# Optimization experiments

Measured on AMD Instinct MI355X. Metric: run time of the kernel, lower is better.

Reference implementation:

```python
import jax, jax.numpy as jnp
import numpy as np
import math

B = 2
LAYERS = 18
LATENT = 512
MAPPER_LAYER = 7  # w_code_num[attention_layer=11]
CLUSTERS = 10
CLUSTER_LAYER = 11
CLUSTER_DIM = 512 + 2 * (512 // 16)  # 576
LR_MUL = 0.1
LAYER_NUM = [0, 2, 3, 5, 6, 8, 9, 11, 12, 14, 15, 17, 18, 20, 21, 23, 24]
CH = [512] * 11 + [256] * 2 + [128] * 3 + [64] * 3 + [32] * 3 + [16] * 3
RES = [4, 8, 8, 16, 16, 32, 32, 64, 64, 128, 128] + [256] * 14


def _forward(x, fmaps, mw, mb, afw, afb, aw, ab, alw, alb, initial_state):
    batch = x.shape[0]
    blend = fmaps[CLUSTER_LAYER - 1]
    size = blend.shape[2]  # 128

    # ---- cluster assignment (torch.no_grad block) ----
    pc = blend.shape[1] // 16  # position_channel = 32
    coords = jnp.arange(size, dtype=jnp.float32) * (2.0 / (size - 1)) - 1.0
    xp = jnp.broadcast_to(coords[None, :], (size, size))
    yp = jnp.broadcast_to(coords[:, None], (size, size))
    cf = jnp.concatenate([
        blend,
        jnp.broadcast_to(xp[None, None], (batch, pc, size, size)),
        jnp.broadcast_to(yp[None, None], (batch, pc, size, size)),
    ], axis=1)
    cf = jax.lax.stop_gradient(cf)
    flat = cf.transpose(0, 2, 3, 1).reshape(-1, cf.shape[1])  # [B*S*S, 576]
    dis = (jnp.sum(flat * flat, axis=1, keepdims=True)
           - 2.0 * flat @ initial_state.T
           + jnp.sum(initial_state * initial_state, axis=1)[None, :])
    assign = jnp.argmin(dis, axis=1).reshape(batch, size, size)
    choice = jnp.arange(batch)[:, None, None] * CLUSTERS + assign  # [B,S,S]

    x7 = x[:, :MAPPER_LAYER, -LATENT:]
    h = x7 * jax.lax.rsqrt(jnp.mean(x7 * x7, axis=-1, keepdims=True) + 1e-8)
    w_scale = (1.0 / math.sqrt(LATENT)) * LR_MUL
    for i in range(3):
        h = jnp.einsum('bci,coi->bco', h, mw[:, i]) * w_scale
        h = jax.nn.leaky_relu(h + mb[:, i][None] * LR_MUL, 0.2) * math.sqrt(2.0)
    delta_zs = jnp.concatenate(
        [h, jnp.zeros((batch, LAYERS - MAPPER_LAYER, LATENT), h.dtype)], axis=1)
    loss_delta = jnp.mean(jnp.sqrt(jnp.sum(delta_zs[:, :MAPPER_LAYER] ** 2, axis=-1)))

    # ---- attention branch (EqualConv2d 1x1 + nearest interpolate, torch semantics) ----
    def conv1x1(f, w, b):
        cin = f.shape[1]
        return jnp.einsum('bihw,oi->bohw', f, w) * (1.0 / math.sqrt(cin)) + b[None, :, None, None]

    def interp(f):  # torch nearest: src = floor(i * in / out)
        H = f.shape[2]
        idx = (jnp.arange(size) * H) // size
        return f[:, :, idx][:, :, :, idx]

    att = [interp(conv1x1(fmaps[-1], afw, afb))]
    for c in range(LAYERS - 1):
        f = fmaps[LAYER_NUM[c]]
        att.append(interp(conv1x1(f, aw[c][:, :f.shape[1]], ab[c])))
    amap = jnp.concatenate(att, axis=1)  # [B, 32*18, S, S]
    logits = jnp.einsum('bihw,i->bhw', amap, alw) * (1.0 / math.sqrt(32 * LAYERS)) + alb[0]
    each = jax.nn.sigmoid(logits)  # [B,S,S]

    # ---- training branch: per-(batch,cluster) masked mean -> segment mean ----
    nseg = batch * CLUSTERS
    seg = choice.reshape(-1)
    vals = each.reshape(-1)
    sums = jax.ops.segment_sum(vals, seg, num_segments=nseg)
    cnts = jax.ops.segment_sum(jnp.ones_like(vals), seg, num_segments=nseg)
    mean = sums / jnp.maximum(cnts, 1.0)
    attention_map = jnp.where(cnts > 0, mean, 1.0)[choice]  # [B,S,S]
    loss_reg = jnp.sum(jnp.where(cnts > 0, jnp.maximum(mean - 0.8, 0.0), 0.0)) / batch
    loss_tv = jnp.mean((each - jax.lax.stop_gradient(attention_map)) ** 2)

    am = attention_map[:, None]  # [B,1,S,S]
    final = jnp.where(am < 0.8, am - jax.lax.stop_gradient(am), am)
    # torchvision gaussian_blur(k=5): sigma = 0.3*((5-1)*0.5-1)+0.8 = 1.1, reflect pad
    xs = jnp.linspace(-2.0, 2.0, 5)
    k1 = jnp.exp(-0.5 * (xs / 1.1) ** 2)
    k1 = k1 / jnp.sum(k1)
    k2 = jnp.outer(k1, k1)[None, None]  # [1,1,5,5]
    padded = jnp.pad(final, ((0, 0), (0, 0), (2, 2), (2, 2)), mode='reflect')
    blurred = jax.lax.conv_general_dilated(padded, k2.astype(final.dtype), (1, 1), 'VALID')
    return delta_zs, blurred, loss_delta, loss_reg, loss_tv


def setup_inputs() -> dict:
    key = jax.random.key(0)
    ks = jax.random.split(key, 40)
    inp = {}
    inp['x'] = jax.random.normal(ks[0], (B, LAYERS, LATENT), jnp.float32)
    for i in range(25):
        inp[f'fmap_{i}'] = jax.random.normal(ks[1 + i], (B, CH[i], RES[i], RES[i]), jnp.float32)
    inp['fmap_25'] = jax.random.normal(ks[26], (B, 512, 4, 4), jnp.float32)
    inp['mw'] = jax.random.normal(ks[27], (MAPPER_LAYER, 3, LATENT, LATENT), jnp.float32)
    inp['mb'] = 0.1 * jax.random.normal(ks[28], (MAPPER_LAYER, 3, LATENT), jnp.float32)
    inp['afw'] = jax.random.normal(ks[29], (32, 512), jnp.float32)
    inp['afb'] = 0.1 * jax.random.normal(ks[30], (32,), jnp.float32)
    inp['aw'] = jax.random.normal(ks[31], (LAYERS - 1, 32, 512), jnp.float32)
    inp['ab'] = 0.1 * jax.random.normal(ks[32], (LAYERS - 1, 32), jnp.float32)
    inp['alw'] = jax.random.normal(ks[33], (32 * LAYERS,), jnp.float32)
    inp['alb'] = jnp.full((1,), 5.0, jnp.float32)  # attention_last bias init to 5
    inp['initial_state'] = jax.random.normal(ks[34], (CLUSTERS, CLUSTER_DIM), jnp.float32)
    inp['size'] = 128
    return inp


def reference(x, fmap_0, fmap_1, fmap_2, fmap_3, fmap_4, fmap_5, fmap_6, fmap_7,
              fmap_8, fmap_9, fmap_10, fmap_11, fmap_12, fmap_13, fmap_14, fmap_15,
              fmap_16, fmap_17, fmap_18, fmap_19, fmap_20, fmap_21, fmap_22, fmap_23,
              fmap_24, fmap_25, mw, mb, afw, afb, aw, ab, alw, alb, initial_state, size):
    fmaps = [fmap_0, fmap_1, fmap_2, fmap_3, fmap_4, fmap_5, fmap_6, fmap_7, fmap_8,
             fmap_9, fmap_10, fmap_11, fmap_12, fmap_13, fmap_14, fmap_15, fmap_16,
             fmap_17, fmap_18, fmap_19, fmap_20, fmap_21, fmap_22, fmap_23, fmap_24,
             fmap_25]
    return _forward(x, fmaps, mw, mb, afw, afb, aw, ab, alw, alb, initial_state)
```

## Files before the change

### kernel.cpp

```cpp
#include <hip/hip_runtime.h>
#include <math.h>

#define NPIX 32768
#define OUT_DZ 0
#define OUT_BLUR 18432
#define OUT_LD 51200
#define OUT_REG 51201
#define OUT_TV 51202
#define NSLAB 48

__constant__ int d_cin[18] = {512,512,512,512,512,512,512,512,256,256,128,128,64,64,32,32,16,16};
__constant__ int d_H[18]   = {4,  4,  8,  16, 32, 32, 64, 128,256,256,256,256,256,256,256,256,256,256};

__constant__ int d_slab_t[NSLAB]  = {0,1,2,3,4,5, 6,6,
                                     7,7,7,7,7,7,7,7,
                                     8,8,8,8,8,8,8,8,
                                     9,9,9,9,9,9,9,9,
                                     10,10,10,10, 11,11,11,11,
                                     12,12, 13,13, 14, 15, 16, 17};
__constant__ int d_slab_c0[NSLAB] = {0,0,0,0,0,0, 0,256,
                                     0,64,128,192,256,320,384,448,
                                     0,32,64,96,128,160,192,224,
                                     0,32,64,96,128,160,192,224,
                                     0,32,64,96, 0,32,64,96,
                                     0,32, 0,32, 0, 0, 0, 0};
__constant__ int d_slab_nc[NSLAB] = {512,512,512,512,512,512, 256,256,
                                     64,64,64,64,64,64,64,64,
                                     32,32,32,32,32,32,32,32,
                                     32,32,32,32,32,32,32,32,
                                     32,32,32,32, 32,32,32,32,
                                     32,32, 32,32, 32, 32, 16, 16};

struct FPtrs { const float* f[18]; };

#define WS_HA     0
#define WS_HB     7168
#define WS_ST     14336
#define WS_CN     22528
#define WS_BIASP  22576
#define WS_V      22656
#define WS_CHOICE 31872
#define WS_PART   64640
#define WS_EACH   1637504
#define WS_SUMS   1670272
#define WS_CNTS   1672832
#define WS_ATTV   1675392
#define WS_TVP    1675424

__global__ __launch_bounds__(512) void k_vfold(
    const float* __restrict__ afw, const float* __restrict__ afb,
    const float* __restrict__ aw,  const float* __restrict__ ab,
    const float* __restrict__ alw, const float* __restrict__ istate,
    float* __restrict__ v, float* __restrict__ biasp,
    float* __restrict__ st, float* __restrict__ cn)
{
    int t = blockIdx.x;
    if (t < 18) {
        int cin = d_cin[t];
        const float* w  = (t==0) ? afw : aw + (size_t)(t-1)*32*512;
        const float* bb = (t==0) ? afb : ab + (t-1)*32;
        float scale = (1.0f/sqrtf((float)cin)) * (1.0f/24.0f);
        int c = threadIdx.x;
        if (c < cin) {
            float s = 0.0f;
            #pragma unroll 8
            for (int o = 0; o < 32; o++) s += alw[t*32+o] * w[o*512 + c];
            v[t*512 + c] = s * scale;
        }
        if (threadIdx.x == 0) {
            float s = 0.0f;
            for (int o = 0; o < 32; o++) s += alw[t*32+o] * bb[o];
            biasp[t] = s * (1.0f/24.0f);
        }
    } else {
        int c = threadIdx.x;
        if (c < 512) {
            #pragma unroll
            for (int j = 0; j < 10; j++) st[c*16 + j] = -2.0f * istate[j*576 + c];
        }
        if (c < 10) {
            int j = c;
            float n = 0.0f, s1 = 0.0f, s2 = 0.0f;
            for (int k = 0; k < 576; k++) { float sv = istate[j*576+k]; n += sv*sv; }
            for (int k = 512; k < 544; k++) s1 += istate[j*576+k];
            for (int k = 544; k < 576; k++) s2 += istate[j*576+k];
            cn[j] = n; cn[16+j] = -2.0f*s1; cn[32+j] = -2.0f*s2;
        }
    }
}

__global__ __launch_bounds__(512, 4) void k_assign(
    const float* __restrict__ blend, const float* __restrict__ st,
    const float* __restrict__ cn, int* __restrict__ choice)
{
    __shared__ float gsh[8*128*10];
    int tid = threadIdx.x;
    int w = tid >> 6, lane = tid & 63;
    int csub = __builtin_amdgcn_readfirstlane(w);
    int pw = blockIdx.x * 128;
    int b = pw >> 14, rem = pw & 16383;
    const float* src = blend + ((size_t)b*512 + csub*64)*16384 + rem + 2*lane;
    const float* stc = st + csub*64*16;
    float g0[10] = {0,0,0,0,0,0,0,0,0,0};
    float g1[10] = {0,0,0,0,0,0,0,0,0,0};
    for (int c0 = 0; c0 < 64; c0 += 4) {
        float2 q[4];
        #pragma unroll
        for (int u = 0; u < 4; u++) q[u] = *(const float2*)(src + (size_t)(c0+u)*16384);
        #pragma unroll
        for (int u = 0; u < 4; u++) {
            #pragma unroll
            for (int j = 0; j < 10; j++) {
                float sv = stc[(c0+u)*16 + j];
                g0[j] = fmaf(q[u].x, sv, g0[j]);
                g1[j] = fmaf(q[u].y, sv, g1[j]);
            }
        }
    }
    #pragma unroll
    for (int j = 0; j < 10; j++) {
        gsh[(w*128 + 2*lane)*10 + j]     = g0[j];
        gsh[(w*128 + 2*lane + 1)*10 + j] = g1[j];
    }
    __syncthreads();
    if (tid < 128) {
        int p = pw + tid;
        int bb = p >> 14, rr = p & 16383, y = rr >> 7, x = rr & 127;
        float cx = (float)x * (float)(2.0/127.0) - 1.0f;
        float cy = (float)y * (float)(2.0/127.0) - 1.0f;
        float gt[10];
        #pragma unroll
        for (int j = 0; j < 10; j++) {
            float acc = cn[j] + cn[16+j]*cx + cn[32+j]*cy;
            #pragma unroll
            for (int ww = 0; ww < 8; ww++) acc += gsh[(ww*128 + tid)*10 + j];
            gt[j] = acc;
        }
        int best = 0; float bg = gt[0];
        #pragma unroll
        for (int j = 1; j < 10; j++) if (gt[j] < bg) { bg = gt[j]; best = j; }
        choice[p] = bb*10 + best;
    }
}

__global__ __launch_bounds__(256) void k_norm(const float* __restrict__ x, float* __restrict__ h)
{
    int r = blockIdx.x;
    int b = r / 7, c = r % 7;
    const float* xr = x + ((size_t)b*18 + c)*512;
    int tid = threadIdx.x;
    float v0 = xr[tid], v1 = xr[tid+256];
    __shared__ float red[256];
    __shared__ float scale;
    red[tid] = v0*v0 + v1*v1; __syncthreads();
    for (int s = 128; s; s >>= 1) { if (tid < s) red[tid] += red[tid+s]; __syncthreads(); }
    if (tid == 0) scale = 1.0f / sqrtf(red[0]*(1.0f/512.0f) + 1e-8f);
    __syncthreads();
    h[r*512 + tid] = v0*scale; h[r*512 + 256 + tid] = v1*scale;
}

__global__ __launch_bounds__(256) void k_mlp(
    const float* __restrict__ mw, const float* __restrict__ mb,
    const float* __restrict__ hin, float* __restrict__ hout,
    int layer, float* __restrict__ dz)
{
    int wave = blockIdx.x*4 + (threadIdx.x >> 6);
    int lane = threadIdx.x & 63;
    int c = wave >> 9, o = wave & 511;
    const float* wrow = mw + (((size_t)(c*3 + layer)*512 + o) << 9) + lane*8;
    float4 w0 = *(const float4*)wrow;
    float4 w1 = *(const float4*)(wrow + 4);
    const float* h0 = hin + (size_t)c*512 + lane*8;
    const float* h1 = hin + (size_t)(7 + c)*512 + lane*8;
    float4 a0 = *(const float4*)h0, a1 = *(const float4*)(h0+4);
    float4 b0 = *(const float4*)h1, b1 = *(const float4*)(h1+4);
    float d0 = a0.x*w0.x + a0.y*w0.y + a0.z*w0.z + a0.w*w0.w
             + a1.x*w1.x + a1.y*w1.y + a1.z*w1.z + a1.w*w1.w;
    float d1 = b0.x*w0.x + b0.y*w0.y + b0.z*w0.z + b0.w*w0.w
             + b1.x*w1.x + b1.y*w1.y + b1.z*w1.z + b1.w*w1.w;
    #pragma unroll
    for (int m = 32; m; m >>= 1) { d0 += __shfl_xor(d0, m); d1 += __shfl_xor(d1, m); }
    if (lane == 0) {
        const float wsc = (float)(0.1/22.62741699796952);
        const float rt2 = 1.41421356237309515f;
        float bias = mb[(c*3 + layer)*512 + o] * 0.1f;
        float z0 = d0*wsc + bias; z0 = (z0 > 0.0f ? z0 : 0.2f*z0) * rt2;
        float z1 = d1*wsc + bias; z1 = (z1 > 0.0f ? z1 : 0.2f*z1) * rt2;
        hout[(size_t)c*512 + o] = z0;
        hout[(size_t)(7 + c)*512 + o] = z1;
        if (dz) {
            dz[((size_t)0*18 + c)*512 + o] = z0;
            dz[((size_t)1*18 + c)*512 + o] = z1;
        }
    }
}

__global__ __launch_bounds__(256) void k_lossdelta(const float* __restrict__ h, float* __restrict__ outp)
{
    __shared__ float red[256];
    int tid = threadIdx.x;
    float total = 0.0f;
    for (int r = 0; r < 14; r++) {
        float v0 = h[r*512 + tid], v1 = h[r*512 + 256 + tid];
        red[tid] = v0*v0 + v1*v1; __syncthreads();
        for (int s = 128; s; s >>= 1) { if (tid < s) red[tid] += red[tid+s]; __syncthreads(); }
        if (tid == 0) total += sqrtf(red[0]);
        __syncthreads();
    }
    if (tid == 0) outp[0] = total * (1.0f/14.0f);
}

__global__ __launch_bounds__(256) void k_zero(float* __restrict__ out)
{
    int z = blockIdx.x*256 + threadIdx.x;
    if (z < 11264) {
        int b = z / (11*512), rem = z % (11*512);
        out[(size_t)b*18*512 + 7*512 + rem] = 0.0f;
    }
}

__global__ __launch_bounds__(256, 4) void k_each(FPtrs fp, const float* __restrict__ v, float* __restrict__ partial)
{
    __shared__ float vsh[512];
    int bid = blockIdx.x;
    int tid = threadIdx.x;
    int s = (bid < 512) ? (bid >> 6) : (8 + ((bid - 512) >> 4));
    int t  = d_slab_t[s];
    int c0 = d_slab_c0[s];
    int nc = d_slab_nc[s];
    int H  = d_H[t];
    int cin = d_cin[t];
    for (int i = tid; i < nc; i += 256) vsh[i] = v[t*512 + c0 + i];
    __syncthreads();
    int w = tid >> 6, lane = tid & 63;

    if (bid >= 512) {
        int sub = (bid - 512) & 15;
        int b = sub >> 3, rowgrp = sub & 7;
        int y0 = rowgrp*16 + w*4;
        const float* base = fp.f[t] + (size_t)(b*cin + c0) * (size_t)H * (size_t)H;
        float* pout = partial + (size_t)s*NPIX + b*16384;
        if (H == 256) {
            float a[4][2] = {{0,0},{0,0},{0,0},{0,0}};
            const float* srcr[4];
            #pragma unroll
            for (int i = 0; i < 4; i++) srcr[i] = base + (size_t)(2*(y0+i))*256 + 4*lane;
            for (int cc = 0; cc < nc; cc += 2) {
                float4 q[2][4];
                #pragma unroll
                for (int u = 0; u < 2; u++)
                    #pragma unroll
                    for (int i = 0; i < 4; i++)
                        q[u][i] = *(const float4*)(srcr[i] + (size_t)(cc+u)*65536);
                #pragma unroll
                for (int u = 0; u < 2; u++) {
                    float vv = vsh[cc+u];
                    #pragma unroll
                    for (int i = 0; i < 4; i++) {
                        a[i][0] = fmaf(q[u][i].x, vv, a[i][0]);
                        a[i][1] = fmaf(q[u][i].z, vv, a[i][1]);
                    }
                }
            }
            #pragma unroll
            for (int i = 0; i < 4; i++) {
                float2 o; o.x = a[i][0]; o.y = a[i][1];
                *(float2*)(pout + (y0+i)*128 + 2*lane) = o;
            }
        } else {
            int h = lane >> 5, c4 = 4*(lane & 31);
            float aA[4] = {0,0,0,0}, aB[4] = {0,0,0,0};
            const float* srcA = base + (size_t)(y0 + h)*128 + c4;
            const float* srcB = base + (size_t)(y0 + 2 + h)*128 + c4;
            for (int cc = 0; cc < nc; cc += 4) {
                float4 qa[4], qb[4];
                #pragma unroll
                for (int u = 0; u < 4; u++) {
                    qa[u] = *(const float4*)(srcA + (size_t)(cc+u)*16384);
                    qb[u] = *(const float4*)(srcB + (size_t)(cc+u)*16384);
                }
                #pragma unroll
                for (int u = 0; u < 4; u++) {
                    float vv = vsh[cc+u];
                    aA[0] = fmaf(qa[u].x, vv, aA[0]); aA[1] = fmaf(qa[u].y, vv, aA[1]);
                    aA[2] = fmaf(qa[u].z, vv, aA[2]); aA[3] = fmaf(qa[u].w, vv, aA[3]);
                    aB[0] = fmaf(qb[u].x, vv, aB[0]); aB[1] = fmaf(qb[u].y, vv, aB[1]);
                    aB[2] = fmaf(qb[u].z, vv, aB[2]); aB[3] = fmaf(qb[u].w, vv, aB[3]);
                }
            }
            float4 oA; oA.x=aA[0]; oA.y=aA[1]; oA.z=aA[2]; oA.w=aA[3];
            float4 oB; oB.x=aB[0]; oB.y=aB[1]; oB.z=aB[2]; oB.w=aB[3];
            *(float4*)(pout + (y0+h)*128 + c4) = oA;
            *(float4*)(pout + (y0+2+h)*128 + c4) = oB;
        }
        return;
    }

    int px = bid & 63;
    int row = w, pbase = px*512;
    int b = pbase >> 14;
    int y = ((pbase & 16383) >> 7) + row;
    const float* base = fp.f[t] + (size_t)(b*cin + c0) * (size_t)(H*H);
    float a0 = 0.0f, a1 = 0.0f;
    if (H == 64) {
        const float* src = base + (size_t)(y >> 1)*64 + lane;
        for (int cc = 0; cc < nc; cc += 8) {
            float q[8];
            #pragma unroll
            for (int u = 0; u < 8; u++) q[u] = src[(size_t)(cc+u)*4096];
            #pragma unroll
            for (int u = 0; u < 8; u++) {
                float vv = vsh[cc+u];
                a0 = fmaf(q[u], vv, a0); a1 = fmaf(q[u], vv, a1);
            }
        }
    } else {
        int x0 = 2*lane, x1 = 2*lane + 1;
        int sy = (y*H) >> 7, sx0 = (x0*H) >> 7, sx1 = (x1*H) >> 7;
        const float* src = base + (size_t)sy*H;
        size_t HH = (size_t)H*H;
        for (int cc = 0; cc < nc; cc += 8) {
            float q0[8], q1[8];
            #pragma unroll
            for (int u = 0; u < 8; u++) {
                q0[u] = src[(size_t)(cc+u)*HH + sx0];
                q1[u] = src[(size_t)(cc+u)*HH + sx1];
            }
            #pragma unroll
            for (int u = 0; u < 8; u++) {
                float vv = vsh[cc+u];
                a0 = fmaf(q0[u], vv, a0); a1 = fmaf(q1[u], vv, a1);
            }
        }
    }
    int p = pbase + row*128 + 2*lane;
    float2 o; o.x = a0; o.y = a1;
    *(float2*)(partial + (size_t)s*NPIX + p) = o;
}

__global__ __launch_bounds__(256) void k_logits(
    const float* __restrict__ partial, const float* __restrict__ biasp,
    const float* __restrict__ alb, const int* __restrict__ choice,
    float* __restrict__ each, float* __restrict__ bsums, int* __restrict__ bcnts)
{
    __shared__ float ssum[20]; __shared__ int scnt[20]; __shared__ float sbias;
    int tid = threadIdx.x;
    if (tid < 20) { ssum[tid] = 0.0f; scnt[tid] = 0; }
    if (tid == 0) {
        float s = alb[0];
        for (int t = 0; t < 18; t++) s += biasp[t];
        sbias = s;
    }
    __syncthreads();
    int p = blockIdx.x*256 + tid;
    float lg = sbias;
    #pragma unroll 8
    for (int s = 0; s < NSLAB; s++) lg += partial[(size_t)s*NPIX + p];
    float e = 1.0f / (1.0f + expf(-lg));
    each[p] = e;
    int ch = choice[p];
    atomicAdd(&ssum[ch], e);
    atomicAdd(&scnt[ch], 1);
    __syncthreads();
    if (tid < 20) { bsums[blockIdx.x*20 + tid] = ssum[tid]; bcnts[blockIdx.x*20 + tid] = scnt[tid]; }
}

__global__ __launch_bounds__(64) void k_stats(
    const float* __restrict__ bsums, const int* __restrict__ bcnts,
    float* __restrict__ attv, float* __restrict__ out)
{
    __shared__ float red[32];
    int j = threadIdx.x;
    float regj = 0.0f;
    if (j < 20) {
        float s = 0.0f; int c = 0;
        for (int blk = 0; blk < 128; blk++) { s += bsums[blk*20 + j]; c += bcnts[blk*20 + j]; }
        float mean = s / fmaxf((float)c, 1.0f);
        attv[j] = (c > 0) ? mean : 1.0f;
        regj = (c > 0) ? fmaxf(mean - 0.8f, 0.0f) : 0.0f;
    }
    if (j < 32) red[j] = (j < 20) ? regj : 0.0f;
    __syncthreads();
    for (int s = 16; s; s >>= 1) { if (j < s) red[j] += red[j+s]; __syncthreads(); }
    if (j == 0) out[OUT_REG] = red[0] * 0.5f;
}

__global__ __launch_bounds__(256) void k_final(
    const float* __restrict__ each, const int* __restrict__ choice,
    const float* __restrict__ attv, float* __restrict__ tvp, float* __restrict__ out)
{
    __shared__ float av[20];
    __shared__ float red[256];
    int tid = threadIdx.x;
    if (tid < 20) av[tid] = attv[tid];
    __syncthreads();
    int p = blockIdx.x*256 + tid;
    int b = p >> 14, rem = p & 16383, y = rem >> 7, x = rem & 127;
    float k1[5]; float ks = 0.0f;
    #pragma unroll
    for (int i = 0; i < 5; i++) { float d = (float)(i-2) / 1.1f; k1[i] = expf(-0.5f*d*d); ks += k1[i]; }
    #pragma unroll
    for (int i = 0; i < 5; i++) k1[i] /= ks;
    const int* cb = choice + b*16384;
    float acc = 0.0f;
    #pragma unroll
    for (int a = 0; a < 5; a++) {
        int yy = y + a - 2; yy = (yy < 0) ? -yy : ((yy > 127) ? 254 - yy : yy);
        #pragma unroll
        for (int bb = 0; bb < 5; bb++) {
            int xx = x + bb - 2; xx = (xx < 0) ? -xx : ((xx > 127) ? 254 - xx : xx);
            float am = av[cb[yy*128 + xx]];
            float fin = (am < 0.8f) ? 0.0f : am;
            acc += k1[a]*k1[bb]*fin;
        }
    }
    out[OUT_BLUR + p] = acc;
    float amc = av[cb[y*128 + x]];
    float d = each[p] - amc;
    red[tid] = d*d; __syncthreads();
    for (int s = 128; s; s >>= 1) { if (tid < s) red[tid] += red[tid+s]; __syncthreads(); }
    if (tid == 0) tvp[blockIdx.x] = red[0];
}

__global__ __launch_bounds__(128) void k_tvred(const float* __restrict__ tvp, float* __restrict__ out)
{
    __shared__ float red[128];
    int tid = threadIdx.x;
    red[tid] = tvp[tid]; __syncthreads();
    for (int s = 64; s; s >>= 1) { if (tid < s) red[tid] += red[tid+s]; __syncthreads(); }
    if (tid == 0) out[OUT_TV] = red[0] * (1.0f/32768.0f);
}

extern "C" void kernel_launch(void* const* d_in, const int* in_sizes, int n_in,
                              void* d_out, int out_size, void* d_ws, size_t ws_size,
                              hipStream_t stream)
{
    const float* x      = (const float*)d_in[0];
    const float* blend  = (const float*)d_in[11];
    const float* mw     = (const float*)d_in[27];
    const float* mb     = (const float*)d_in[28];
    const float* afw    = (const float*)d_in[29];
    const float* afb    = (const float*)d_in[30];
    const float* aw     = (const float*)d_in[31];
    const float* ab     = (const float*)d_in[32];
    const float* alw    = (const float*)d_in[33];
    const float* alb    = (const float*)d_in[34];
    const float* istate = (const float*)d_in[35];
    float* out = (float*)d_out;
    float* ws  = (float*)d_ws;

    static const int LN[17] = {0,2,3,5,6,8,9,11,12,14,15,17,18,20,21,23,24};
    FPtrs fp;
    fp.f[0] = (const float*)d_in[26];
    for (int c = 0; c < 17; c++) fp.f[1+c] = (const float*)d_in[1 + LN[c]];

    float* hA     = ws + WS_HA;
    float* hB     = ws + WS_HB;
    float* st     = ws + WS_ST;
    float* cn     = ws + WS_CN;
    float* biasp  = ws + WS_BIASP;
    float* v      = ws + WS_V;
    int*   choice = (int*)(ws + WS_CHOICE);
    float* part   = ws + WS_PART;
    float* each   = ws + WS_EACH;
    float* bsums  = ws + WS_SUMS;
    int*   bcnts  = (int*)(ws + WS_CNTS);
    float* attv   = ws + WS_ATTV;
    float* tvp    = ws + WS_TVP;

    k_vfold<<<dim3(19), 512, 0, stream>>>(afw, afb, aw, ab, alw, istate, v, biasp, st, cn);
    k_norm<<<14, 256, 0, stream>>>(x, hA);
    k_mlp<<<896, 256, 0, stream>>>(mw, mb, hA, hB, 0, nullptr);
    k_mlp<<<896, 256, 0, stream>>>(mw, mb, hB, hA, 1, nullptr);
    k_mlp<<<896, 256, 0, stream>>>(mw, mb, hA, hB, 2, out + OUT_DZ);
    k_lossdelta<<<1, 256, 0, stream>>>(hB, out + OUT_LD);
    k_zero<<<44, 256, 0, stream>>>(out);
    k_assign<<<256, 512, 0, stream>>>(blend, st, cn, choice);
    k_each<<<512 + (NSLAB-8)*16, 256, 0, stream>>>(fp, v, part);
    k_logits<<<128, 256, 0, stream>>>(part, biasp, alb, choice, each, bsums, bcnts);
    k_stats<<<1, 64, 0, stream>>>(bsums, bcnts, attv, out);
    k_final<<<128, 256, 0, stream>>>(each, choice, attv, tvp, out);
    k_tvred<<<1, 128, 0, stream>>>(tvp, out);
}
```

Measured before the change: 163.5 us.

## Split attention reduction into heavy and light kernels with in-block channel reduction

Replaces the single slab-based k_each kernel with two kernels. k_heavy handles layers 7-17: each 512-thread block covers one 512-pixel tile, its 8 waves stride over channels with software-prefetched loads, and the per-wave sums are reduced in shared memory. k_light handles layers 0-6. Partial buffers drop from 48 slabs to 18, which shrinks the workspace and the k_logits summation. The cost is one extra kernel launch, fewer blocks for the heavy layers, and only one load in flight per wave per step.

```diff
diff --git a/kernel.cpp b/kernel.cpp
--- a/kernel.cpp
+++ b/kernel.cpp
@@ -7,29 +7,9 @@
 #define OUT_LD 51200
 #define OUT_REG 51201
 #define OUT_TV 51202
-#define NSLAB 48
 
 __constant__ int d_cin[18] = {512,512,512,512,512,512,512,512,256,256,128,128,64,64,32,32,16,16};
 __constant__ int d_H[18]   = {4,  4,  8,  16, 32, 32, 64, 128,256,256,256,256,256,256,256,256,256,256};
-
-__constant__ int d_slab_t[NSLAB]  = {0,1,2,3,4,5, 6,6,
-                                     7,7,7,7,7,7,7,7,
-                                     8,8,8,8,8,8,8,8,
-                                     9,9,9,9,9,9,9,9,
-                                     10,10,10,10, 11,11,11,11,
-                                     12,12, 13,13, 14, 15, 16, 17};
-__constant__ int d_slab_c0[NSLAB] = {0,0,0,0,0,0, 0,256,
-                                     0,64,128,192,256,320,384,448,
-                                     0,32,64,96,128,160,192,224,
-                                     0,32,64,96,128,160,192,224,
-                                     0,32,64,96, 0,32,64,96,
-                                     0,32, 0,32, 0, 0, 0, 0};
-__constant__ int d_slab_nc[NSLAB] = {512,512,512,512,512,512, 256,256,
-                                     64,64,64,64,64,64,64,64,
-                                     32,32,32,32,32,32,32,32,
-                                     32,32,32,32,32,32,32,32,
-                                     32,32,32,32, 32,32,32,32,
-                                     32,32, 32,32, 32, 32, 16, 16};
 
 struct FPtrs { const float* f[18]; };
 
@@ -41,11 +21,11 @@
 #define WS_V      22656
 #define WS_CHOICE 31872
 #define WS_PART   64640
-#define WS_EACH   1637504
-#define WS_SUMS   1670272
-#define WS_CNTS   1672832
-#define WS_ATTV   1675392
-#define WS_TVP    1675424
+#define WS_EACH   654464
+#define WS_SUMS   687232
+#define WS_CNTS   689792
+#define WS_ATTV   692352
+#define WS_TVP    692384
 
 __global__ __launch_bounds__(512) void k_vfold(
     const float* __restrict__ afw, const float* __restrict__ afb,
@@ -219,88 +199,108 @@
     }
 }
 
-__global__ __launch_bounds__(256, 4) void k_each(FPtrs fp, const float* __restrict__ v, float* __restrict__ partial)
+__global__ __launch_bounds__(512) void k_heavy(FPtrs fp, const float* __restrict__ v, float* __restrict__ partial)
+{
+    __shared__ float gsh[8*512];
+    int bid = blockIdx.x;
+    int t  = 7 + (bid >> 6);
+    int b  = (bid >> 5) & 1;
+    int rb = bid & 31;
+    int ch = d_cin[t];
+    int H  = d_H[t];
+    int w = threadIdx.x >> 6, lane = threadIdx.x & 63;
+    const float* vt = v + t*512;
+    const float* base0 = fp.f[t] + (size_t)b*ch*(size_t)H*H;
+    float2 a0={0,0}, a1={0,0}, a2={0,0}, a3={0,0};
+
+    if (H == 256) {
+        const float* srcw = base0 + (size_t)rb*2048 + 4*lane;
+        int c = w;
+        const float* sA = srcw + (size_t)c*65536;
+        float4 p0 = *(const float4*)(sA);
+        float4 p1 = *(const float4*)(sA + 512);
+        float4 p2 = *(const float4*)(sA + 1024);
+        float4 p3 = *(const float4*)(sA + 1536);
+        while (c + 8 < ch) {
+            int cn_ = c + 8;
+            const float* sB = srcw + (size_t)cn_*65536;
+            float4 n0 = *(const float4*)(sB);
+            float4 n1 = *(const float4*)(sB + 512);
+            float4 n2 = *(const float4*)(sB + 1024);
+            float4 n3 = *(const float4*)(sB + 1536);
+            float vv = vt[c];
+            a0.x = fmaf(p0.x, vv, a0.x); a0.y = fmaf(p0.z, vv, a0.y);
+            a1.x = fmaf(p1.x, vv, a1.x); a1.y = fmaf(p1.z, vv, a1.y);
+            a2.x = fmaf(p2.x, vv, a2.x); a2.y = fmaf(p2.z, vv, a2.y);
+            a3.x = fmaf(p3.x, vv, a3.x); a3.y = fmaf(p3.z, vv, a3.y);
+            p0 = n0; p1 = n1; p2 = n2; p3 = n3;
+            c = cn_;
+        }
+        float vv = vt[c];
+        a0.x = fmaf(p0.x, vv, a0.x); a0.y = fmaf(p0.z, vv, a0.y);
+        a1.x = fmaf(p1.x, vv, a1.x); a1.y = fmaf(p1.z, vv, a1.y);
+        a2.x = fmaf(p2.x, vv, a2.x); a2.y = fmaf(p2.z, vv, a2.y);
+        a3.x = fmaf(p3.x, vv, a3.x); a3.y = fmaf(p3.z, vv, a3.y);
+    } else {
+        const float* srcw = base0 + (size_t)rb*512 + 2*lane;
+        int c = w;
+        const float* sA = srcw + (size_t)c*16384;
+        float2 p0 = *(const float2*)(sA);
+        float2 p1 = *(const float2*)(sA + 128);
+        float2 p2 = *(const float2*)(sA + 256);
+        float2 p3 = *(const float2*)(sA + 384);
+        while (c + 8 < ch) {
+            int cn_ = c + 8;
+            const float* sB = srcw + (size_t)cn_*16384;
+            float2 n0 = *(const float2*)(sB);
+            float2 n1 = *(const float2*)(sB + 128);
+            float2 n2 = *(const float2*)(sB + 256);
+            float2 n3 = *(const float2*)(sB + 384);
+            float vv = vt[c];
+            a0.x = fmaf(p0.x, vv, a0.x); a0.y = fmaf(p0.y, vv, a0.y);
+            a1.x = fmaf(p1.x, vv, a1.x); a1.y = fmaf(p1.y, vv, a1.y);
+            a2.x = fmaf(p2.x, vv, a2.x); a2.y = fmaf(p2.y, vv, a2.y);
+            a3.x = fmaf(p3.x, vv, a3.x); a3.y = fmaf(p3.y, vv, a3.y);
+            p0 = n0; p1 = n1; p2 = n2; p3 = n3;
+            c = cn_;
+        }
+        float vv = vt[c];
+        a0.x = fmaf(p0.x, vv, a0.x); a0.y = fmaf(p0.y, vv, a0.y);
+        a1.x = fmaf(p1.x, vv, a1.x); a1.y = fmaf(p1.y, vv, a1.y);
+        a2.x = fmaf(p2.x, vv, a2.x); a2.y = fmaf(p2.y, vv, a2.y);
+        a3.x = fmaf(p3.x, vv, a3.x); a3.y = fmaf(p3.y, vv, a3.y);
+    }
+    {
+        float* gw = gsh + w*512 + 2*lane;
+        *(float2*)(gw)       = a0;
+        *(float2*)(gw + 128) = a1;
+        *(float2*)(gw + 256) = a2;
+        *(float2*)(gw + 384) = a3;
+    }
+    __syncthreads();
+    int idx = threadIdx.x;
+    float s = 0.0f;
+    #pragma unroll
+    for (int ww = 0; ww < 8; ww++) s += gsh[ww*512 + idx];
+    partial[(size_t)t*NPIX + b*16384 + rb*512 + idx] = s;
+}
+
+__global__ __launch_bounds__(256) void k_light(FPtrs fp, const float* __restrict__ v, float* __restrict__ partial)
 {
     __shared__ float vsh[512];
     int bid = blockIdx.x;
     int tid = threadIdx.x;
-    int s = (bid < 512) ? (bid >> 6) : (8 + ((bid - 512) >> 4));
-    int t  = d_slab_t[s];
-    int c0 = d_slab_c0[s];
-    int nc = d_slab_nc[s];
+    int t  = bid >> 6;
+    int nc = d_cin[t];
     int H  = d_H[t];
-    int cin = d_cin[t];
-    for (int i = tid; i < nc; i += 256) vsh[i] = v[t*512 + c0 + i];
+    for (int i = tid; i < nc; i += 256) vsh[i] = v[t*512 + i];
     __syncthreads();
     int w = tid >> 6, lane = tid & 63;
-
-    if (bid >= 512) {
-        int sub = (bid - 512) & 15;
-        int b = sub >> 3, rowgrp = sub & 7;
-        int y0 = rowgrp*16 + w*4;
-        const float* base = fp.f[t] + (size_t)(b*cin + c0) * (size_t)H * (size_t)H;
-        float* pout = partial + (size_t)s*NPIX + b*16384;
-        if (H == 256) {
-            float a[4][2] = {{0,0},{0,0},{0,0},{0,0}};
-            const float* srcr[4];
-            #pragma unroll
-            for (int i = 0; i < 4; i++) srcr[i] = base + (size_t)(2*(y0+i))*256 + 4*lane;
-            for (int cc = 0; cc < nc; cc += 2) {
-                float4 q[2][4];
-                #pragma unroll
-                for (int u = 0; u < 2; u++)
-                    #pragma unroll
-                    for (int i = 0; i < 4; i++)
-                        q[u][i] = *(const float4*)(srcr[i] + (size_t)(cc+u)*65536);
-                #pragma unroll
-                for (int u = 0; u < 2; u++) {
-                    float vv = vsh[cc+u];
-                    #pragma unroll
-                    for (int i = 0; i < 4; i++) {
-                        a[i][0] = fmaf(q[u][i].x, vv, a[i][0]);
-                        a[i][1] = fmaf(q[u][i].z, vv, a[i][1]);
-                    }
-                }
-            }
-            #pragma unroll
-            for (int i = 0; i < 4; i++) {
-                float2 o; o.x = a[i][0]; o.y = a[i][1];
-                *(float2*)(pout + (y0+i)*128 + 2*lane) = o;
-            }
-        } else {
-            int h = lane >> 5, c4 = 4*(lane & 31);
-            float aA[4] = {0,0,0,0}, aB[4] = {0,0,0,0};
-            const float* srcA = base + (size_t)(y0 + h)*128 + c4;
-            const float* srcB = base + (size_t)(y0 + 2 + h)*128 + c4;
-            for (int cc = 0; cc < nc; cc += 4) {
-                float4 qa[4], qb[4];
-                #pragma unroll
-                for (int u = 0; u < 4; u++) {
-                    qa[u] = *(const float4*)(srcA + (size_t)(cc+u)*16384);
-                    qb[u] = *(const float4*)(srcB + (size_t)(cc+u)*16384);
-                }
-                #pragma unroll
-                for (int u = 0; u < 4; u++) {
-                    float vv = vsh[cc+u];
-                    aA[0] = fmaf(qa[u].x, vv, aA[0]); aA[1] = fmaf(qa[u].y, vv, aA[1]);
-                    aA[2] = fmaf(qa[u].z, vv, aA[2]); aA[3] = fmaf(qa[u].w, vv, aA[3]);
-                    aB[0] = fmaf(qb[u].x, vv, aB[0]); aB[1] = fmaf(qb[u].y, vv, aB[1]);
-                    aB[2] = fmaf(qb[u].z, vv, aB[2]); aB[3] = fmaf(qb[u].w, vv, aB[3]);
-                }
-            }
-            float4 oA; oA.x=aA[0]; oA.y=aA[1]; oA.z=aA[2]; oA.w=aA[3];
-            float4 oB; oB.x=aB[0]; oB.y=aB[1]; oB.z=aB[2]; oB.w=aB[3];
-            *(float4*)(pout + (y0+h)*128 + c4) = oA;
-            *(float4*)(pout + (y0+2+h)*128 + c4) = oB;
-        }
-        return;
-    }
-
     int px = bid & 63;
-    int row = w, pbase = px*512;
+    int pbase = px*512;
     int b = pbase >> 14;
-    int y = ((pbase & 16383) >> 7) + row;
-    const float* base = fp.f[t] + (size_t)(b*cin + c0) * (size_t)(H*H);
+    int y = ((pbase & 16383) >> 7) + w;
+    const float* base = fp.f[t] + (size_t)b*nc*(size_t)(H*H);
     float a0 = 0.0f, a1 = 0.0f;
     if (H == 64) {
         const float* src = base + (size_t)(y >> 1)*64 + lane;
@@ -333,9 +333,9 @@
             }
         }
     }
-    int p = pbase + row*128 + 2*lane;
+    int p = pbase + w*128 + 2*lane;
     float2 o; o.x = a0; o.y = a1;
-    *(float2*)(partial + (size_t)s*NPIX + p) = o;
+    *(float2*)(partial + (size_t)t*NPIX + p) = o;
 }
 
 __global__ __launch_bounds__(256) void k_logits(
@@ -354,8 +354,8 @@
     __syncthreads();
     int p = blockIdx.x*256 + tid;
     float lg = sbias;
-    #pragma unroll 8
-    for (int s = 0; s < NSLAB; s++) lg += partial[(size_t)s*NPIX + p];
+    #pragma unroll
+    for (int s = 0; s < 18; s++) lg += partial[(size_t)s*NPIX + p];
     float e = 1.0f / (1.0f + expf(-lg));
     each[p] = e;
     int ch = choice[p];
@@ -476,7 +476,8 @@
     k_lossdelta<<<1, 256, 0, stream>>>(hB, out + OUT_LD);
     k_zero<<<44, 256, 0, stream>>>(out);
     k_assign<<<256, 512, 0, stream>>>(blend, st, cn, choice);
-    k_each<<<512 + (NSLAB-8)*16, 256, 0, stream>>>(fp, v, part);
+    k_heavy<<<11*64, 512, 0, stream>>>(fp, v, part);
+    k_light<<<7*64, 256, 0, stream>>>(fp, v, part);
     k_logits<<<128, 256, 0, stream>>>(part, biasp, alb, choice, each, bsums, bcnts);
     k_stats<<<1, 64, 0, stream>>>(bsums, bcnts, attv, out);
     k_final<<<128, 256, 0, stream>>>(each, choice, attv, tvp, out);
```

New measurement: 182.0 us. +11.3%, slower.
